# Kernel optimization log

Hardware: AMD Instinct MI355X
Metric: run time of the kernel (lower is better)

## Reference

```python
import jax, jax.numpy as jnp
import numpy as np

N_NODES = 100000
N_EDGES = 600000
IN_DIM = 128
EDGE_DIM = 32
HIDDEN = 128
NUM_CLASSES = 2


def _glorot(key, shape):
    fan_in, fan_out = shape[0], shape[1]
    lim = float(np.sqrt(6.0 / (fan_in + fan_out)))
    return jax.random.uniform(key, shape, jnp.float32, -lim, lim)


def setup_inputs() -> dict:
    key = jax.random.key(0)
    ks = jax.random.split(key, 16)
    inp = {
        "x": jax.random.normal(ks[0], (N_NODES, IN_DIM), jnp.float32),
        "edge_index": jax.random.randint(ks[1], (2, N_EDGES), 0, N_NODES, jnp.int64),
        "edge_attr": jax.random.normal(ks[2], (N_EDGES, EDGE_DIM), jnp.float32),
        # SAGEConv layer 1 (edge-aware): edge proj, neighbor lin, self lin
        "We1": _glorot(ks[3], (EDGE_DIM, IN_DIM)),
        "be1": jnp.zeros((IN_DIM,), jnp.float32),
        "Wl1": _glorot(ks[4], (IN_DIM, HIDDEN)),
        "bl1": jnp.zeros((HIDDEN,), jnp.float32),
        "Wr1": _glorot(ks[5], (IN_DIM, HIDDEN)),
        "br1": jnp.zeros((HIDDEN,), jnp.float32),
        # SAGEConv layer 2
        "We2": _glorot(ks[6], (EDGE_DIM, HIDDEN)),
        "be2": jnp.zeros((HIDDEN,), jnp.float32),
        "Wl2": _glorot(ks[7], (HIDDEN, HIDDEN)),
        "bl2": jnp.zeros((HIDDEN,), jnp.float32),
        "Wr2": _glorot(ks[8], (HIDDEN, HIDDEN)),
        "br2": jnp.zeros((HIDDEN,), jnp.float32),
        # Edge MLP predictor: Linear(2*hidden, hidden) -> ReLU -> Linear(hidden, num_classes)
        "Wp1": _glorot(ks[9], (2 * HIDDEN, HIDDEN)),
        "bp1": jnp.zeros((HIDDEN,), jnp.float32),
        "Wp2": _glorot(ks[10], (HIDDEN, NUM_CLASSES)),
        "bp2": jnp.zeros((NUM_CLASSES,), jnp.float32),
    }
    return inp


def _sage_conv(x, src, dst, edge_attr, We, be, Wl, bl, Wr, br):
    # Edge-aware message: m_ij = x_j + proj(e_ij); mean-aggregate over dst;
    # out_i = mean_agg @ Wl + x_i @ Wr  (GraphSAGE mean aggregator with edge fusion)
    msg = x[src] + edge_attr @ We + be                       # [E, d]
    agg = jax.ops.segment_sum(msg, dst, num_segments=N_NODES)  # [N, d]
    deg = jax.ops.segment_sum(jnp.ones((msg.shape[0],), msg.dtype), dst, num_segments=N_NODES)
    mean = agg / jnp.maximum(deg, 1.0)[:, None]
    return mean @ Wl + bl + x @ Wr + br


def reference(x, edge_index, edge_attr,
              We1, be1, Wl1, bl1, Wr1, br1,
              We2, be2, Wl2, bl2, Wr2, br2,
              Wp1, bp1, Wp2, bp2):
    src, dst = edge_index[0], edge_index[1]
    h = jax.nn.relu(_sage_conv(x, src, dst, edge_attr, We1, be1, Wl1, bl1, Wr1, br1))
    h = jax.nn.relu(_sage_conv(h, src, dst, edge_attr, We2, be2, Wl2, bl2, Wr2, br2))
    # Edge predictor: gather endpoints, concat, MLP -> logits [E, num_classes]
    he = jnp.concatenate([h[src], h[dst]], axis=-1)
    return jax.nn.relu(he @ Wp1 + bp1) @ Wp2 + bp2
```

## Files before the change

### kernel.cpp

```cpp
#include <hip/hip_runtime.h>

#define N_NODES 100000
#define N_EDGES 600000
#define IN_DIM 128
#define EDGE_DIM 32
#define HIDDEN 128
#define NUM_CLASSES 2
#define NBLK 391

typedef __attribute__((ext_vector_type(4))) float f32x4;
typedef _Float16 f16x2 __attribute__((ext_vector_type(2)));
typedef _Float16 f16x4 __attribute__((ext_vector_type(4)));
typedef _Float16 f16x8 __attribute__((ext_vector_type(8)));

__global__ void hist_kernel(const int* __restrict__ dst, int* __restrict__ cnt) {
    int e = blockIdx.x * blockDim.x + threadIdx.x;
    if (e < N_EDGES) atomicAdd(&cnt[dst[e]], 1);
}

__global__ void scan1_kernel(const int* __restrict__ cnt,
                             int* __restrict__ scanout, int* __restrict__ bsum) {
    __shared__ int s[256];
    int tid = threadIdx.x;
    int i = blockIdx.x * 256 + tid;
    int v = (i < N_NODES) ? cnt[i] : 0;
    s[tid] = v;
    __syncthreads();
#pragma unroll
    for (int off = 1; off < 256; off <<= 1) {
        int t = 0;
        if (tid >= off) t = s[tid - off];
        __syncthreads();
        if (tid >= off) s[tid] += t;
        __syncthreads();
    }
    if (i < N_NODES) scanout[i] = s[tid];
    if (tid == 255) bsum[blockIdx.x] = s[255];
}

__global__ void scan2_kernel(int* __restrict__ bsum) {
    __shared__ int s[512];
    int tid = threadIdx.x;
    int v = (tid < NBLK) ? bsum[tid] : 0;
    s[tid] = v;
    __syncthreads();
#pragma unroll
    for (int off = 1; off < 512; off <<= 1) {
        int t = 0;
        if (tid >= off) t = s[tid - off];
        __syncthreads();
        if (tid >= off) s[tid] += t;
        __syncthreads();
    }
    if (tid < NBLK) bsum[tid] = s[tid] - v;
}

__global__ void scan3_kernel(const int* __restrict__ cnt,
                             const int* __restrict__ scanout,
                             const int* __restrict__ bsum,
                             int* __restrict__ rowptr, int* __restrict__ cur) {
    int i = blockIdx.x * 256 + threadIdx.x;
    if (i < N_NODES) {
        int excl = scanout[i] + bsum[i >> 8] - cnt[i];
        rowptr[i] = excl;
        cur[i] = excl;
    }
    if (i == 0) rowptr[N_NODES] = N_EDGES;
}

__global__ void fill_kernel(const int* __restrict__ src, const int* __restrict__ dst,
                            int* __restrict__ cur, int2* __restrict__ pk,
                            int* __restrict__ pdst) {
    int e = blockIdx.x * blockDim.x + threadIdx.x;
    if (e < N_EDGES) {
        int d = dst[e];
        int pos = atomicAdd(&cur[d], 1);
        int2 v;
        v.x = src[e];
        v.y = e;
        pk[pos] = v;
        pdst[pos] = d;
    }
}

__global__ void xb_kernel(const float* __restrict__ x, _Float16* __restrict__ xb) {
    int i = blockIdx.x * 256 + threadIdx.x;
    if (i < N_NODES * HIDDEN / 2) {
        float2 v = ((const float2*)x)[i];
        f16x2 o;
        o.x = (_Float16)v.x;
        o.y = (_Float16)v.y;
        *(f16x2*)&xb[i * 2] = o;
    }
}

__global__ void wewl2_kernel(const float* __restrict__ We1, const float* __restrict__ be1,
                             const float* __restrict__ Wl1,
                             const float* __restrict__ We2, const float* __restrict__ be2,
                             const float* __restrict__ Wl2,
                             float* __restrict__ WeWl1, float* __restrict__ beWl1,
                             float* __restrict__ WeWl2, float* __restrict__ beWl2) {
    int idx0 = blockIdx.x * 256 + threadIdx.x;
    if (idx0 >= 2 * 33 * 128) return;
    int layer = idx0 >= 33 * 128;
    int idx = idx0 - layer * 33 * 128;
    const float* We = layer ? We2 : We1;
    const float* be = layer ? be2 : be1;
    const float* Wl = layer ? Wl2 : Wl1;
    float* WeWl = layer ? WeWl2 : WeWl1;
    float* beWl = layer ? beWl2 : beWl1;
    int r = idx >> 7;
    int n = idx & 127;
    float s = 0.f;
    if (r < 32) {
        for (int j = 0; j < 128; ++j) s += We[r * 128 + j] * Wl[j * 128 + n];
        WeWl[r * 128 + n] = s;
    } else {
        for (int j = 0; j < 128; ++j) s += be[j] * Wl[j * 128 + n];
        beWl[n] = s;
    }
}

__global__ void wbig2_kernel(const float* __restrict__ Wl1, const float* __restrict__ Wr1,
                             const float* __restrict__ WeWl1, _Float16* __restrict__ Wbs1,
                             const float* __restrict__ Wl2, const float* __restrict__ Wr2,
                             const float* __restrict__ WeWl2, _Float16* __restrict__ Wbs2) {
    int idx0 = blockIdx.x * 256 + threadIdx.x;
    if (idx0 >= 2 * 36864) return;
    int layer = idx0 >= 36864;
    int idx = idx0 - layer * 36864;
    const float* Wl = layer ? Wl2 : Wl1;
    const float* Wr = layer ? Wr2 : Wr1;
    const float* WeWl = layer ? WeWl2 : WeWl1;
    _Float16* Wbs = layer ? Wbs2 : Wbs1;
    int j = idx & 7;
    int lane = (idx >> 3) & 63;
    int rem = idx >> 9;
    int ks = rem % 9;
    int nt = rem / 9;
    int k = ks * 32 + ((lane >> 4) & 3) * 8 + j;
    int n = nt * 16 + (lane & 15);
    float v = (k < 128) ? Wl[k * 128 + n]
            : (k < 256) ? Wr[(k - 128) * 128 + n]
                        : WeWl[(k - 256) * 128 + n];
    Wbs[idx] = (_Float16)v;
}

template <bool EA>
__global__ __launch_bounds__(256) void agg_kernel_t(const _Float16* __restrict__ xin,
                                                    const int* __restrict__ rowptr,
                                                    const int2* __restrict__ pk,
                                                    const float* __restrict__ ea,
                                                    _Float16* __restrict__ meanb,
                                                    _Float16* __restrict__ eamb) {
    int wid = blockIdx.x * 4 + (threadIdx.x >> 6);
    int lane = threadIdx.x & 63;
    int node = lane >> 3;
    int slot = lane & 7;
    int half = lane >> 5;
    int l32 = lane & 31;
    int n0 = wid * 8;

    int rp = rowptr[n0 + (lane < 9 ? lane : 8)];
    int s_n = __shfl(rp, node);
    int e_n = __shfl(rp, node + 1);
    int c_n = e_n - s_n; c_n = c_n > 8 ? 8 : c_n;
    int pos = s_n + (slot < c_n ? slot : 0);
    pos = pos < N_EDGES ? pos : N_EDGES - 1;
    int2 pv = pk[pos];

#pragma unroll 1
    for (int g = 0; g < 2; ++g) {
        float ax[4][4];
        float eacc[4];
#pragma unroll
        for (int i = 0; i < 4; ++i) {
            ax[i][0] = 0.f; ax[i][1] = 0.f; ax[i][2] = 0.f; ax[i][3] = 0.f;
            if (EA) eacc[i] = 0.f;
        }

#pragma unroll
        for (int i = 0; i < 4; ++i) {
            int ni = g * 4 + i;
            int di = __shfl(rp, ni + 1) - __shfl(rp, ni);
            int ci = di > 8 ? 8 : di;
            f16x4 r[4];
#pragma unroll
            for (int u = 0; u < 4; ++u) {
                int s = __shfl(pv.x, ni * 8 + 2 * u + half);
                r[u] = *(const f16x4*)&xin[s * HIDDEN + l32 * 4];
            }
            float gg[4];
            if (EA) {
#pragma unroll
                for (int u = 0; u < 4; ++u) {
                    int eid = __shfl(pv.y, ni * 8 + 2 * u + half);
                    gg[u] = ea[eid * EDGE_DIM + l32];
                }
            }
#pragma unroll
            for (int u = 0; u < 4; ++u) {
                if (2 * u + half < ci) {
                    ax[i][0] += (float)r[u].x; ax[i][1] += (float)r[u].y;
                    ax[i][2] += (float)r[u].z; ax[i][3] += (float)r[u].w;
                    if (EA) eacc[i] += gg[u];
                }
            }
        }

#pragma unroll
        for (int i = 0; i < 4; ++i) {
            int ni = g * 4 + i;
            int si = __shfl(rp, ni);
            int ei = __shfl(rp, ni + 1);
            int p = si + 8;
            if (p < ei) {
                do {
                    int c = ei - p; c = c > 8 ? 8 : c;
                    int2 pv2 = pk[p + (slot < c ? slot : 0)];
                    f16x4 r[4];
#pragma unroll
                    for (int u = 0; u < 4; ++u) {
                        int s = __shfl(pv2.x, 2 * u + half);
                        r[u] = *(const f16x4*)&xin[s * HIDDEN + l32 * 4];
                    }
                    float gg[4];
                    if (EA) {
#pragma unroll
                        for (int u = 0; u < 4; ++u) {
                            int eid = __shfl(pv2.y, 2 * u + half);
                            gg[u] = ea[eid * EDGE_DIM + l32];
                        }
                    }
#pragma unroll
                    for (int u = 0; u < 4; ++u) {
                        if (2 * u + half < c) {
                            ax[i][0] += (float)r[u].x; ax[i][1] += (float)r[u].y;
                            ax[i][2] += (float)r[u].z; ax[i][3] += (float)r[u].w;
                            if (EA) eacc[i] += gg[u];
                        }
                    }
                    p += c;
                } while (p < ei);
            }
        }

        float dinv[4];
#pragma unroll
        for (int i = 0; i < 4; ++i) {
            int ni = g * 4 + i;
            int di = __shfl(rp, ni + 1) - __shfl(rp, ni);
            dinv[i] = 1.f / (float)(di > 1 ? di : 1);
#pragma unroll
            for (int c = 0; c < 4; ++c) ax[i][c] += __shfl_xor(ax[i][c], 32);
            if (EA) eacc[i] += __shfl_xor(eacc[i], 32);
        }
#pragma unroll
        for (int j = 0; j < 2; ++j) {
            float v0 = half ? ax[2 * j + 1][0] : ax[2 * j][0];
            float v1 = half ? ax[2 * j + 1][1] : ax[2 * j][1];
            float v2 = half ? ax[2 * j + 1][2] : ax[2 * j][2];
            float v3 = half ? ax[2 * j + 1][3] : ax[2 * j][3];
            float dv = half ? dinv[2 * j + 1] : dinv[2 * j];
            int nw = n0 + g * 4 + 2 * j + half;
            f16x4 o;
            o.x = (_Float16)(v0 * dv); o.y = (_Float16)(v1 * dv);
            o.z = (_Float16)(v2 * dv); o.w = (_Float16)(v3 * dv);
            *(f16x4*)&meanb[nw * HIDDEN + l32 * 4] = o;
            if (EA) {
                float ev = half ? eacc[2 * j + 1] : eacc[2 * j];
                eamb[nw * EDGE_DIM + l32] = (_Float16)(ev * dv);
            }
        }
    }
}

#define APITCH 296
__global__ __launch_bounds__(256) void node_gemm_kernel(
        const _Float16* __restrict__ meanb,
        const _Float16* __restrict__ xb,
        const _Float16* __restrict__ eamb,
        const _Float16* __restrict__ Wbs,
        const int* __restrict__ rowptr,
        const float* __restrict__ bl, const float* __restrict__ br,
        const float* __restrict__ beWl,
        _Float16* __restrict__ outb) {
    __shared__ _Float16 s_a[64 * APITCH];
    __shared__ float s_bias[128];
    __shared__ float s_bw[128];
    __shared__ int s_deg[64];
    int t = threadIdx.x;
    int n0 = blockIdx.x * 64;

    if (t < 128) {
        s_bias[t] = bl[t] + br[t];
        s_bw[t] = beWl[t];
    } else if (t < 192) {
        int m = t - 128;
        int n = n0 + m;
        n = n < N_NODES ? n : N_NODES - 1;
        s_deg[m] = rowptr[n + 1] - rowptr[n];
    }
    for (int i = t; i < 64 * 16; i += 256) {
        int row = i >> 4, seg = i & 15;
        int n = n0 + row;
        n = n < N_NODES ? n : N_NODES - 1;
        *(f16x8*)&s_a[row * APITCH + seg * 8] = *(const f16x8*)&meanb[n * HIDDEN + seg * 8];
        *(f16x8*)&s_a[row * APITCH + 128 + seg * 8] = *(const f16x8*)&xb[n * HIDDEN + seg * 8];
    }
    for (int i = t; i < 64 * 4; i += 256) {
        int row = i >> 2, seg = i & 3;
        int n = n0 + row;
        n = n < N_NODES ? n : N_NODES - 1;
        *(f16x8*)&s_a[row * APITCH + 256 + seg * 8] = *(const f16x8*)&eamb[n * EDGE_DIM + seg * 8];
    }
    __syncthreads();

    int wave = t >> 6;
    int lane = t & 63;
    int col = lane & 15;
    int kgrp = lane >> 4;

    f32x4 acc[4][2];
#pragma unroll
    for (int rt = 0; rt < 4; ++rt) {
        acc[rt][0] = (f32x4){0.f, 0.f, 0.f, 0.f};
        acc[rt][1] = (f32x4){0.f, 0.f, 0.f, 0.f};
    }

    const f16x8* __restrict__ Wb = (const f16x8*)Wbs;
#pragma unroll
    for (int ks = 0; ks < 9; ++ks) {
        f16x8 b0 = Wb[((2 * wave + 0) * 9 + ks) * 64 + lane];
        f16x8 b1 = Wb[((2 * wave + 1) * 9 + ks) * 64 + lane];
#pragma unroll
        for (int rt = 0; rt < 4; ++rt) {
            f16x8 afrag = *(const f16x8*)&s_a[(rt * 16 + col) * APITCH + ks * 32 + kgrp * 8];
            acc[rt][0] = __builtin_amdgcn_mfma_f32_16x16x32_f16(afrag, b0, acc[rt][0], 0, 0, 0);
            acc[rt][1] = __builtin_amdgcn_mfma_f32_16x16x32_f16(afrag, b1, acc[rt][1], 0, 0, 0);
        }
    }

#pragma unroll
    for (int rt = 0; rt < 4; ++rt) {
#pragma unroll
        for (int j = 0; j < 2; ++j) {
            int feat = (2 * wave + j) * 16 + col;
            float b = s_bias[feat];
            float bw = s_bw[feat];
#pragma unroll
            for (int r = 0; r < 4; ++r) {
                int m = rt * 16 + kgrp * 4 + r;
                int n = n0 + m;
                float v = acc[rt][j][r] + b + (s_deg[m] > 0 ? bw : 0.f);
                v = v > 0.f ? v : 0.f;
                if (n < N_NODES) outb[n * HIDDEN + feat] = (_Float16)v;
            }
        }
    }
}

__global__ void wp1uv_swizzle_kernel(const float* __restrict__ Wp1,
                                     const float* __restrict__ Wp2,
                                     _Float16* __restrict__ Wuv,
                                     _Float16* __restrict__ Wp2b) {
    int idx = blockIdx.x * 256 + threadIdx.x;
    if (idx < 32768) {
        int j = idx & 7;
        int lane = (idx >> 3) & 63;
        int ks = (idx >> 9) & 3;
        int nt = (idx >> 11) & 15;
        int k = ks * 32 + ((lane >> 4) & 3) * 8 + j;
        int n = nt * 16 + (lane & 15);
        float v = (n < 128) ? Wp1[k * 128 + n] : Wp1[(128 + k) * 128 + (n - 128)];
        Wuv[idx] = (_Float16)v;
    } else if (idx < 32768 + 2048) {
        int r = idx - 32768;
        int j = r & 7;
        int lane = (r >> 3) & 63;
        int ks = r >> 9;
        int k = ks * 32 + ((lane >> 4) & 3) * 8 + j;
        int col = lane & 15;
        Wp2b[r] = (col < 2) ? (_Float16)Wp2[k * 2 + col] : (_Float16)0;
    }
}

#define UPITCH 136
__global__ __launch_bounds__(256) void uv_gemm_kernel(
        const _Float16* __restrict__ h,
        const _Float16* __restrict__ Wuv,
        const float* __restrict__ bp1,
        _Float16* __restrict__ UV) {
    __shared__ _Float16 s_a[64 * UPITCH];
    __shared__ float s_bias[256];
    int t = threadIdx.x;
    int n0 = blockIdx.x * 64;

    s_bias[t] = (t < 128) ? bp1[t] : 0.f;
    for (int i = t; i < 64 * 16; i += 256) {
        int row = i >> 4, seg = i & 15;
        int n = n0 + row;
        n = n < N_NODES ? n : N_NODES - 1;
        *(f16x8*)&s_a[row * UPITCH + seg * 8] = *(const f16x8*)&h[n * HIDDEN + seg * 8];
    }
    __syncthreads();

    int wave = t >> 6;
    int lane = t & 63;
    int col = lane & 15;
    int kgrp = lane >> 4;

    f32x4 acc[4][4];
#pragma unroll
    for (int rt = 0; rt < 4; ++rt)
#pragma unroll
        for (int j = 0; j < 4; ++j) acc[rt][j] = (f32x4){0.f, 0.f, 0.f, 0.f};

    const f16x8* __restrict__ Wb = (const f16x8*)Wuv;
#pragma unroll
    for (int ks = 0; ks < 4; ++ks) {
        f16x8 bf[4];
#pragma unroll
        for (int j = 0; j < 4; ++j)
            bf[j] = Wb[((4 * wave + j) * 4 + ks) * 64 + lane];
#pragma unroll
        for (int rt = 0; rt < 4; ++rt) {
            f16x8 afrag = *(const f16x8*)&s_a[(rt * 16 + col) * UPITCH + ks * 32 + kgrp * 8];
#pragma unroll
            for (int j = 0; j < 4; ++j)
                acc[rt][j] = __builtin_amdgcn_mfma_f32_16x16x32_f16(afrag, bf[j], acc[rt][j], 0, 0, 0);
        }
    }

#pragma unroll
    for (int rt = 0; rt < 4; ++rt) {
#pragma unroll
        for (int j = 0; j < 4; ++j) {
            int feat = (4 * wave + j) * 16 + col;
            float b = s_bias[feat];
#pragma unroll
            for (int r = 0; r < 4; ++r) {
                int m = rt * 16 + kgrp * 4 + r;
                int n = n0 + m;
                if (n < N_NODES) UV[n * 256 + feat] = (_Float16)(acc[rt][j][r] + b);
            }
        }
    }
}

__global__ __launch_bounds__(256) void edge_pred_kernel(
        const _Float16* __restrict__ UV,
        const int2* __restrict__ pk,
        const int* __restrict__ pdst,
        const _Float16* __restrict__ Wp2b,
        const float* __restrict__ bp2,
        float* __restrict__ out) {
    int t = threadIdx.x;
    int wave = t >> 6;
    int lane = t & 63;
    int row = lane & 15;
    int kgrp = lane >> 4;
    int e0 = blockIdx.x * 64 + wave * 16;

    int2 pv = pk[e0 + row];
    int dn = pdst[e0 + row];
    const _Float16* ubase = &UV[pv.x * 256 + kgrp * 8];
    const _Float16* vbase = &UV[dn * 256 + 128 + kgrp * 8];

    f16x8 au[4], av[4], bf[4];
#pragma unroll
    for (int ks = 0; ks < 4; ++ks) {
        au[ks] = *(const f16x8*)&ubase[ks * 32];
        av[ks] = *(const f16x8*)&vbase[ks * 32];
        bf[ks] = *(const f16x8*)&Wp2b[(ks * 64 + lane) * 8];
    }

    f32x4 acc = (f32x4){0.f, 0.f, 0.f, 0.f};
#pragma unroll
    for (int ks = 0; ks < 4; ++ks) {
        f16x8 z = au[ks] + av[ks];
#pragma unroll
        for (int j = 0; j < 8; ++j) z[j] = z[j] > (_Float16)0 ? z[j] : (_Float16)0;
        acc = __builtin_amdgcn_mfma_f32_16x16x32_f16(z, bf[ks], acc, 0, 0, 0);
    }

    int eids[4];
#pragma unroll
    for (int r = 0; r < 4; ++r) eids[r] = __shfl(pv.y, kgrp * 4 + r);

    int col = lane & 15;
    if (col < 2) {
        float bb = bp2[col];
#pragma unroll
        for (int r = 0; r < 4; ++r) out[eids[r] * 2 + col] = acc[r] + bb;
    }
}

extern "C" void kernel_launch(void* const* d_in, const int* in_sizes, int n_in,
                              void* d_out, int out_size, void* d_ws, size_t ws_size,
                              hipStream_t stream) {
    const float* x   = (const float*)d_in[0];
    const int*   ei  = (const int*)d_in[1];
    const float* ea  = (const float*)d_in[2];
    const float* We1 = (const float*)d_in[3];
    const float* be1 = (const float*)d_in[4];
    const float* Wl1 = (const float*)d_in[5];
    const float* bl1 = (const float*)d_in[6];
    const float* Wr1 = (const float*)d_in[7];
    const float* br1 = (const float*)d_in[8];
    const float* We2 = (const float*)d_in[9];
    const float* be2 = (const float*)d_in[10];
    const float* Wl2 = (const float*)d_in[11];
    const float* bl2 = (const float*)d_in[12];
    const float* Wr2 = (const float*)d_in[13];
    const float* br2 = (const float*)d_in[14];
    const float* Wp1 = (const float*)d_in[15];
    const float* bp1 = (const float*)d_in[16];
    const float* Wp2 = (const float*)d_in[17];
    const float* bp2 = (const float*)d_in[18];
    float* out = (float*)d_out;

    const int* src = ei;
    const int* dst = ei + N_EDGES;

    char* ws = (char*)d_ws;
    int*   cnt     = (int*)(ws + 0);
    int*   scanout = (int*)(ws + 409600);
    int*   bsum    = (int*)(ws + 819200);
    int*   rowptr  = (int*)(ws + 827392);
    int*   cur     = (int*)(ws + 1236992);
    int2*  pk      = (int2*)(ws + 1646592);
    float* WeWl1   = (float*)(ws + 6447104);
    float* beWl1   = (float*)(ws + 6463488);
    float* WeWl2   = (float*)(ws + 6464000);
    float* beWl2   = (float*)(ws + 6480384);
    _Float16* eamb = (_Float16*)(ws + 6480896);
    _Float16* xb   = (_Float16*)(ws + 12880896);
    _Float16* meanb= (_Float16*)(ws + 38480896);
    _Float16* UV   = (_Float16*)(ws + 12880896);
    _Float16* h1b  = (_Float16*)(ws + 64080896);
    _Float16* h2b  = (_Float16*)(ws + 89680896);
    _Float16* Wbs1 = (_Float16*)(ws + 115280896);
    _Float16* Wbs2 = (_Float16*)(ws + 115354624);
    _Float16* Wuv  = (_Float16*)(ws + 115428352);
    int*   pdst    = (int*)(ws + 115493888);
    _Float16* Wp2b = (_Float16*)(ws + 409600);

    const int EB = (N_EDGES + 255) / 256;

    hipMemsetAsync(cnt, 0, N_NODES * sizeof(int), stream);
    hist_kernel<<<EB, 256, 0, stream>>>(dst, cnt);
    scan1_kernel<<<NBLK, 256, 0, stream>>>(cnt, scanout, bsum);
    scan2_kernel<<<1, 512, 0, stream>>>(bsum);
    scan3_kernel<<<NBLK, 256, 0, stream>>>(cnt, scanout, bsum, rowptr, cur);
    fill_kernel<<<EB, 256, 0, stream>>>(src, dst, cur, pk, pdst);

    wewl2_kernel<<<33, 256, 0, stream>>>(We1, be1, Wl1, We2, be2, Wl2,
                                         WeWl1, beWl1, WeWl2, beWl2);
    xb_kernel<<<(N_NODES * HIDDEN / 2 + 255) / 256, 256, 0, stream>>>(x, xb);
    wbig2_kernel<<<288, 256, 0, stream>>>(Wl1, Wr1, WeWl1, Wbs1,
                                          Wl2, Wr2, WeWl2, Wbs2);
    wp1uv_swizzle_kernel<<<136, 256, 0, stream>>>(Wp1, Wp2, Wuv, Wp2b);

    agg_kernel_t<true><<<N_NODES / 32, 256, 0, stream>>>(xb, rowptr, pk, ea, meanb, eamb);
    node_gemm_kernel<<<(N_NODES + 63) / 64, 256, 0, stream>>>(
        meanb, xb, eamb, Wbs1, rowptr, bl1, br1, beWl1, h1b);

    agg_kernel_t<false><<<N_NODES / 32, 256, 0, stream>>>(h1b, rowptr, pk, nullptr, meanb, nullptr);
    node_gemm_kernel<<<(N_NODES + 63) / 64, 256, 0, stream>>>(
        meanb, h1b, eamb, Wbs2, rowptr, bl2, br2, beWl2, h2b);

    uv_gemm_kernel<<<(N_NODES + 63) / 64, 256, 0, stream>>>(h2b, Wuv, bp1, UV);
    edge_pred_kernel<<<N_EDGES / 64, 256, 0, stream>>>(UV, pk, pdst, Wp2b, bp2, out);
}
```

Before: 430.3 us.

## Remap aggregation wave to quarter-wave per node pair with 16-byte gathers

Restructures the mean-aggregation kernel so each 16-lane quarter of a wave owns two nodes and reads full 128-wide feature rows as f16x8 (16-byte) loads, instead of half-waves splitting rows with 8-byte loads and a cross-half shuffle reduction. Edge-attribute gathers become float2 loads, and the high-degree tail loop loads edge indices directly in batches of 4 rather than via shuffles. This removes the final shfl_xor reduction and the group loop, and widens memory transactions to cut gather instruction count. The tradeoff is more registers per lane and more serialization for high-degree nodes, since each quarter walks its nodes' tails on its own.

```diff
diff --git a/kernel.cpp b/kernel.cpp
--- a/kernel.cpp
+++ b/kernel.cpp
@@ -157,8 +157,8 @@
     int lane = threadIdx.x & 63;
     int node = lane >> 3;
     int slot = lane & 7;
-    int half = lane >> 5;
-    int l32 = lane & 31;
+    int q = lane >> 4;
+    int l16 = lane & 15;
     int n0 = wid * 8;
 
     int rp = rowptr[n0 + (lane < 9 ? lane : 8)];
@@ -169,108 +169,96 @@
     pos = pos < N_EDGES ? pos : N_EDGES - 1;
     int2 pv = pk[pos];
 
-#pragma unroll 1
-    for (int g = 0; g < 2; ++g) {
-        float ax[4][4];
-        float eacc[4];
-#pragma unroll
-        for (int i = 0; i < 4; ++i) {
-            ax[i][0] = 0.f; ax[i][1] = 0.f; ax[i][2] = 0.f; ax[i][3] = 0.f;
-            if (EA) eacc[i] = 0.f;
-        }
-
-#pragma unroll
-        for (int i = 0; i < 4; ++i) {
-            int ni = g * 4 + i;
-            int di = __shfl(rp, ni + 1) - __shfl(rp, ni);
-            int ci = di > 8 ? 8 : di;
-            f16x4 r[4];
+    float ax[2][8];
+    float ea2[2][2];
+#pragma unroll
+    for (int j = 0; j < 2; ++j) {
+#pragma unroll
+        for (int c = 0; c < 8; ++c) ax[j][c] = 0.f;
+        if (EA) { ea2[j][0] = 0.f; ea2[j][1] = 0.f; }
+    }
+
+    int nj0 = 2 * q;
+    int d0 = __shfl(rp, nj0 + 1) - __shfl(rp, nj0);
+    int d1 = __shfl(rp, nj0 + 2) - __shfl(rp, nj0 + 1);
+
+#pragma unroll
+    for (int j = 0; j < 2; ++j) {
+        int nj = nj0 + j;
+        int dj = j ? d1 : d0;
+        int cj = dj > 8 ? 8 : dj;
+#pragma unroll
+        for (int b = 0; b < 2; ++b) {
+            f16x8 r[4];
+            float2 g[4];
 #pragma unroll
             for (int u = 0; u < 4; ++u) {
-                int s = __shfl(pv.x, ni * 8 + 2 * u + half);
-                r[u] = *(const f16x4*)&xin[s * HIDDEN + l32 * 4];
-            }
-            float gg[4];
+                int s = __shfl(pv.x, nj * 8 + b * 4 + u);
+                r[u] = *(const f16x8*)&xin[s * HIDDEN + l16 * 8];
+            }
             if (EA) {
 #pragma unroll
                 for (int u = 0; u < 4; ++u) {
-                    int eid = __shfl(pv.y, ni * 8 + 2 * u + half);
-                    gg[u] = ea[eid * EDGE_DIM + l32];
+                    int eid = __shfl(pv.y, nj * 8 + b * 4 + u);
+                    g[u] = *(const float2*)&ea[eid * EDGE_DIM + l16 * 2];
                 }
             }
 #pragma unroll
             for (int u = 0; u < 4; ++u) {
-                if (2 * u + half < ci) {
-                    ax[i][0] += (float)r[u].x; ax[i][1] += (float)r[u].y;
-                    ax[i][2] += (float)r[u].z; ax[i][3] += (float)r[u].w;
-                    if (EA) eacc[i] += gg[u];
+                if (b * 4 + u < cj) {
+#pragma unroll
+                    for (int c = 0; c < 8; ++c) ax[j][c] += (float)r[u][c];
+                    if (EA) { ea2[j][0] += g[u].x; ea2[j][1] += g[u].y; }
                 }
             }
         }
-
-#pragma unroll
-        for (int i = 0; i < 4; ++i) {
-            int ni = g * 4 + i;
-            int si = __shfl(rp, ni);
-            int ei = __shfl(rp, ni + 1);
-            int p = si + 8;
-            if (p < ei) {
-                do {
-                    int c = ei - p; c = c > 8 ? 8 : c;
-                    int2 pv2 = pk[p + (slot < c ? slot : 0)];
-                    f16x4 r[4];
-#pragma unroll
-                    for (int u = 0; u < 4; ++u) {
-                        int s = __shfl(pv2.x, 2 * u + half);
-                        r[u] = *(const f16x4*)&xin[s * HIDDEN + l32 * 4];
-                    }
-                    float gg[4];
-                    if (EA) {
-#pragma unroll
-                        for (int u = 0; u < 4; ++u) {
-                            int eid = __shfl(pv2.y, 2 * u + half);
-                            gg[u] = ea[eid * EDGE_DIM + l32];
-                        }
-                    }
-#pragma unroll
-                    for (int u = 0; u < 4; ++u) {
-                        if (2 * u + half < c) {
-                            ax[i][0] += (float)r[u].x; ax[i][1] += (float)r[u].y;
-                            ax[i][2] += (float)r[u].z; ax[i][3] += (float)r[u].w;
-                            if (EA) eacc[i] += gg[u];
-                        }
-                    }
-                    p += c;
-                } while (p < ei);
-            }
-        }
-
-        float dinv[4];
-#pragma unroll
-        for (int i = 0; i < 4; ++i) {
-            int ni = g * 4 + i;
-            int di = __shfl(rp, ni + 1) - __shfl(rp, ni);
-            dinv[i] = 1.f / (float)(di > 1 ? di : 1);
-#pragma unroll
-            for (int c = 0; c < 4; ++c) ax[i][c] += __shfl_xor(ax[i][c], 32);
-            if (EA) eacc[i] += __shfl_xor(eacc[i], 32);
-        }
-#pragma unroll
-        for (int j = 0; j < 2; ++j) {
-            float v0 = half ? ax[2 * j + 1][0] : ax[2 * j][0];
-            float v1 = half ? ax[2 * j + 1][1] : ax[2 * j][1];
-            float v2 = half ? ax[2 * j + 1][2] : ax[2 * j][2];
-            float v3 = half ? ax[2 * j + 1][3] : ax[2 * j][3];
-            float dv = half ? dinv[2 * j + 1] : dinv[2 * j];
-            int nw = n0 + g * 4 + 2 * j + half;
-            f16x4 o;
-            o.x = (_Float16)(v0 * dv); o.y = (_Float16)(v1 * dv);
-            o.z = (_Float16)(v2 * dv); o.w = (_Float16)(v3 * dv);
-            *(f16x4*)&meanb[nw * HIDDEN + l32 * 4] = o;
-            if (EA) {
-                float ev = half ? eacc[2 * j + 1] : eacc[2 * j];
-                eamb[nw * EDGE_DIM + l32] = (_Float16)(ev * dv);
-            }
+    }
+
+#pragma unroll
+    for (int j = 0; j < 2; ++j) {
+        int nj = nj0 + j;
+        int sj = __shfl(rp, nj);
+        int ej = __shfl(rp, nj + 1);
+        int p = sj + 8;
+        while (p < ej) {
+            int c = ej - p; c = c > 4 ? 4 : c;
+            f16x8 r[4];
+            float2 g[4];
+            int2 pv2[4];
+#pragma unroll
+            for (int u = 0; u < 4; ++u)
+                pv2[u] = pk[p + (u < c ? u : 0)];
+#pragma unroll
+            for (int u = 0; u < 4; ++u) {
+                r[u] = *(const f16x8*)&xin[pv2[u].x * HIDDEN + l16 * 8];
+                if (EA) g[u] = *(const float2*)&ea[pv2[u].y * EDGE_DIM + l16 * 2];
+            }
+#pragma unroll
+            for (int u = 0; u < 4; ++u) {
+                if (u < c) {
+#pragma unroll
+                    for (int cc = 0; cc < 8; ++cc) ax[j][cc] += (float)r[u][cc];
+                    if (EA) { ea2[j][0] += g[u].x; ea2[j][1] += g[u].y; }
+                }
+            }
+            p += c;
+        }
+    }
+
+#pragma unroll
+    for (int j = 0; j < 2; ++j) {
+        int nj = nj0 + j;
+        int dj = j ? d1 : d0;
+        float dv = 1.f / (float)(dj > 1 ? dj : 1);
+        f16x8 o;
+#pragma unroll
+        for (int c = 0; c < 8; ++c) o[c] = (_Float16)(ax[j][c] * dv);
+        *(f16x8*)&meanb[(n0 + nj) * HIDDEN + l16 * 8] = o;
+        if (EA) {
+            f16x2 eo;
+            eo.x = (_Float16)(ea2[j][0] * dv);
+            eo.y = (_Float16)(ea2[j][1] * dv);
+            *(f16x2*)&eamb[(n0 + nj) * EDGE_DIM + l16 * 2] = eo;
         }
     }
 }
@@ -536,8 +524,8 @@
     float* beWl2   = (float*)(ws + 6480384);
     _Float16* eamb = (_Float16*)(ws + 6480896);
     _Float16* xb   = (_Float16*)(ws + 12880896);
+    _Float16* UV   = (_Float16*)(ws + 12880896);
     _Float16* meanb= (_Float16*)(ws + 38480896);
-    _Float16* UV   = (_Float16*)(ws + 12880896);
     _Float16* h1b  = (_Float16*)(ws + 64080896);
     _Float16* h2b  = (_Float16*)(ws + 89680896);
     _Float16* Wbs1 = (_Float16*)(ws + 115280896);
```

After: 430.0 us. No clear change (-0.1%).
